# Performance work log

Measured on AMD Instinct MI355X. Metric: run time of the kernel, lower is better.

Reference implementation:

```python
import jax, jax.numpy as jnp
import numpy as np

B, N, E = 2, 4096, 256
H, TAU = 8, 32
HD = E // H
SCALING = HD ** -0.5


def setup_inputs() -> dict:
    key0 = jax.random.key(0)
    kq, kk, kv, kw = jax.random.split(key0, 4)
    return {
        "query": jax.random.normal(kq, (B, N, E), dtype=jnp.float32),
        "key": jax.random.normal(kk, (B, N, E), dtype=jnp.float32),
        "value": jax.random.normal(kv, (B, N, E), dtype=jnp.float32),
        "W": jax.random.normal(kw, (E, E), dtype=jnp.float32) * 0.02,
        "b": jnp.zeros((E,), dtype=jnp.float32),
    }


def reference(query, key, value, W, b):
    b_, n_, e_ = query.shape
    # Zero-pad the front so token i attends to keys/values at positions
    # [i - TAU + 1, ..., i] (sliding causal window of length TAU).
    pad = jnp.zeros((b_, TAU - 1, e_), dtype=query.dtype)
    kp = jnp.concatenate([pad, key], axis=1)   # [B, N+TAU-1, E]
    vp = jnp.concatenate([pad, value], axis=1)
    win_idx = jnp.arange(n_)[:, None] + jnp.arange(TAU)[None, :]  # [N, TAU]
    wk = kp[:, win_idx]  # [B, N, TAU, E] (materialized windows, as torch unfold does)
    wv = vp[:, win_idx]

    proj = lambda x: x @ W.T + b  # shared projection for q, k, v (single nn.Linear)
    q = proj(query).reshape(b_, n_, H, HD)            # [B, N, H, HD]
    k = proj(wk).reshape(b_, n_, TAU, H, HD)          # [B, N, TAU, H, HD]
    v = proj(wv).reshape(b_, n_, TAU, H, HD)

    scores = jnp.einsum("bnhd,bnthd->bhnt", q, k) * SCALING  # [B, H, N, TAU]
    attn = jax.nn.softmax(scores, axis=-1)
    out = jnp.einsum("bhnt,bnthd->bnhd", attn, v)             # [B, N, H, HD]
    return out.reshape(b_, n_, e_)
```

## Files before the change

kernel.cpp:

```cpp
#include <hip/hip_runtime.h>

#define SCALING 0.17677669529663687f

typedef __attribute__((ext_vector_type(8))) short bf8;
typedef __attribute__((ext_vector_type(4))) short bf4;
typedef __attribute__((ext_vector_type(4))) float floatx4;

__device__ __forceinline__ short f2bf(float f) {
    union { float f; unsigned u; } v; v.f = f;
    unsigned u = v.u;
    return (short)((u + 0x7FFFu + ((u >> 16) & 1u)) >> 16);
}
__device__ __forceinline__ float bf2f(short s) {
    union { unsigned u; float f; } v;
    v.u = ((unsigned)(unsigned short)s) << 16;
    return v.f;
}

#define PSTR 264
#define MSTR 36

__global__ __launch_bounds__(512, 2) void fused_kernel(
    const float* __restrict__ q, const float* __restrict__ k,
    const float* __restrict__ v, const float* __restrict__ W,
    const float* __restrict__ bias, float* __restrict__ out)
{
    __shared__ short Pl[160][PSTR];
    __shared__ short As[160][40];
    __shared__ short Bs[256][40];
    __shared__ float Mg[256][MSTR];

    const int tid = threadIdx.x;
    const int n0  = blockIdx.x * 32;
    const int b   = blockIdx.y;
    const int lane = tid & 63, wid = tid >> 6;
    const int wm = wid & 1, wn = wid >> 1;
    const int quad = lane >> 4, l16 = lane & 15;

    int a_row[3]; int a_c4[3]; const float* a_ptr[3];
    #pragma unroll
    for (int i = 0; i < 3; i++) {
        int idx = tid + i * 512;
        if (idx < 1280) {
            int r = idx >> 3;
            a_row[i] = r;
            a_c4[i]  = (idx & 7) * 4;
            const float* p;
            if (r < 32) {
                p = q + (size_t)(b * 4096 + n0 + r) * 256;
            } else if (r < 96) {
                int j = n0 + r - 64;
                p = (j >= 0) ? (k + (size_t)(b * 4096 + j) * 256) : nullptr;
            } else {
                int j = n0 + r - 128;
                p = (j >= 0) ? (v + (size_t)(b * 4096 + j) * 256) : nullptr;
            }
            a_ptr[i] = p;
        } else { a_row[i] = -1; a_c4[i] = 0; a_ptr[i] = nullptr; }
    }
    int w_row[4], w_c4[4];
    #pragma unroll
    for (int i = 0; i < 4; i++) {
        int idx = tid + i * 512;
        w_row[i] = idx >> 3;
        w_c4[i]  = (idx & 7) * 4;
    }

    floatx4 acc[5][4];
    #pragma unroll
    for (int mt = 0; mt < 5; mt++)
        #pragma unroll
        for (int nt = 0; nt < 4; nt++) acc[mt][nt] = (floatx4)0.0f;

    for (int k0 = 0; k0 < 256; k0 += 32) {
        bf4 ab[3];
        #pragma unroll
        for (int i = 0; i < 3; i++) {
            float4 xa = make_float4(0.f, 0.f, 0.f, 0.f);
            if (a_ptr[i]) xa = *(const float4*)(a_ptr[i] + k0 + a_c4[i]);
            ab[i][0] = f2bf(xa.x); ab[i][1] = f2bf(xa.y);
            ab[i][2] = f2bf(xa.z); ab[i][3] = f2bf(xa.w);
        }
        bf4 wb[4];
        #pragma unroll
        for (int i = 0; i < 4; i++) {
            float4 wv = *(const float4*)(W + (size_t)w_row[i] * 256 + k0 + w_c4[i]);
            wb[i][0] = f2bf(wv.x); wb[i][1] = f2bf(wv.y);
            wb[i][2] = f2bf(wv.z); wb[i][3] = f2bf(wv.w);
        }
        __syncthreads();
        #pragma unroll
        for (int i = 0; i < 3; i++)
            if (a_row[i] >= 0) *(bf4*)&As[a_row[i]][a_c4[i]] = ab[i];
        #pragma unroll
        for (int i = 0; i < 4; i++)
            *(bf4*)&Bs[w_row[i]][w_c4[i]] = wb[i];
        __syncthreads();

        bf8 af[5], bfr[4];
        #pragma unroll
        for (int mt = 0; mt < 5; mt++)
            af[mt] = *(const bf8*)&As[wm * 80 + mt * 16 + l16][quad * 8];
        #pragma unroll
        for (int nt = 0; nt < 4; nt++)
            bfr[nt] = *(const bf8*)&Bs[wn * 64 + nt * 16 + l16][quad * 8];
        #pragma unroll
        for (int mt = 0; mt < 5; mt++)
            #pragma unroll
            for (int nt = 0; nt < 4; nt++)
                acc[mt][nt] = __builtin_amdgcn_mfma_f32_16x16x32_bf16(
                    af[mt], bfr[nt], acc[mt][nt], 0, 0, 0);
    }

    #pragma unroll
    for (int nt = 0; nt < 4; nt++) {
        int col = wn * 64 + nt * 16 + l16;
        float bv = bias[col];
        #pragma unroll
        for (int mt = 0; mt < 5; mt++) {
            int rb = wm * 80 + mt * 16 + quad * 4;
            #pragma unroll
            for (int r = 0; r < 4; r++)
                Pl[rb + r][col] = f2bf(acc[mt][nt][r] + bv);
        }
    }
    __syncthreads();

    const int pid  = tid & 255;
    const int half = tid >> 8;
    const int nl   = pid & 31;
    const int h    = pid >> 5;
    const int cb   = h * 32;
    const int t0   = half * 16;

    float qv[32];
    #pragma unroll
    for (int c = 0; c < 4; c++) {
        bf8 t = *(const bf8*)&Pl[nl][cb + c * 8];
        #pragma unroll
        for (int e = 0; e < 8; e++) qv[c * 8 + e] = bf2f(t[e]);
    }

    float s[16], m = -3.0e38f;
    #pragma unroll
    for (int tt = 0; tt < 16; tt++) {
        int r = 33 + nl + t0 + tt;
        float a = 0.f;
        #pragma unroll
        for (int c = 0; c < 4; c++) {
            bf8 kk = *(const bf8*)&Pl[r][cb + c * 8];
            #pragma unroll
            for (int e = 0; e < 8; e++) a += qv[c * 8 + e] * bf2f(kk[e]);
        }
        s[tt] = a * SCALING;
        m = fmaxf(m, s[tt]);
    }
    float l = 0.f;
    #pragma unroll
    for (int tt = 0; tt < 16; tt++) { s[tt] = __expf(s[tt] - m); l += s[tt]; }

    float o[32];
    #pragma unroll
    for (int e = 0; e < 32; e++) o[e] = 0.f;
    #pragma unroll
    for (int tt = 0; tt < 16; tt++) {
        int r = 97 + nl + t0 + tt;
        float a = s[tt];
        #pragma unroll
        for (int c = 0; c < 4; c++) {
            bf8 vv = *(const bf8*)&Pl[r][cb + c * 8];
            #pragma unroll
            for (int e = 0; e < 8; e++) o[c * 8 + e] += a * bf2f(vv[e]);
        }
    }

    if (half == 1) {
        #pragma unroll
        for (int c = 0; c < 16; c++)
            *(float2*)&Mg[pid][c * 2] = make_float2(o[c * 2], o[c * 2 + 1]);
        Mg[pid][32] = m; Mg[pid][33] = l;
    }
    __syncthreads();
    if (half == 0) {
        float m1 = Mg[pid][32], l1 = Mg[pid][33];
        float mm = fmaxf(m, m1);
        float a0 = __expf(m - mm), a1 = __expf(m1 - mm);
        float inv = 1.0f / (a0 * l + a1 * l1);
        #pragma unroll
        for (int c = 0; c < 16; c++) {
            float2 o1 = *(const float2*)&Mg[pid][c * 2];
            float2 r2 = make_float2((a0 * o[c * 2]     + a1 * o1.x) * inv,
                                    (a0 * o[c * 2 + 1] + a1 * o1.y) * inv);
            *(float2*)&Mg[pid][c * 2] = r2;
        }
    }
    __syncthreads();

    const size_t obase = ((size_t)b * 4096 + n0) * 256;
    #pragma unroll
    for (int i = 0; i < 4; i++) {
        int t4   = tid + i * 512;
        int e    = t4 * 4;
        int n    = e >> 8;
        int rest = e & 255;
        int hh   = rest >> 5, cc = rest & 31;
        int pp   = hh * 32 + n;
        float4 val = *(const float4*)&Mg[pp][cc];
        *(float4*)(out + obase + (size_t)n * 256 + rest) = val;
    }
}

extern "C" void kernel_launch(void* const* d_in, const int* in_sizes, int n_in,
                              void* d_out, int out_size, void* d_ws, size_t ws_size,
                              hipStream_t stream) {
    (void)in_sizes; (void)n_in; (void)out_size; (void)d_ws; (void)ws_size;
    const float* q    = (const float*)d_in[0];
    const float* k    = (const float*)d_in[1];
    const float* v    = (const float*)d_in[2];
    const float* W    = (const float*)d_in[3];
    const float* bias = (const float*)d_in[4];
    float* outp = (float*)d_out;

    hipLaunchKernelGGL(fused_kernel, dim3(128, 2), dim3(512), 0, stream,
                       q, k, v, W, bias, outp);
}
```

Baseline: 97.14 us.

## Compute windowed attention scores and PV with MFMA instead of scalar loops

Replaces the per-thread scalar QK dot products and PV accumulation with MFMA tiles per head (one wave per head). Scores are computed as banded 32x64 block products with masking, softmax is reduced via lane shuffles, probabilities are staged in fp16 shared memory, and V is stored transposed in fp16 for an fp16 MFMA. Scaling is folded into Q at projection time and the merge buffer and its syncs are removed. This trades redundant masked MFMA work and an fp16 precision change for far fewer scalar FMAs and LDS reads.

```diff
diff --git a/kernel.cpp b/kernel.cpp
--- a/kernel.cpp
+++ b/kernel.cpp
@@ -4,6 +4,8 @@
 
 typedef __attribute__((ext_vector_type(8))) short bf8;
 typedef __attribute__((ext_vector_type(4))) short bf4;
+typedef _Float16 half8 __attribute__((ext_vector_type(8)));
+typedef _Float16 half4 __attribute__((ext_vector_type(4)));
 typedef __attribute__((ext_vector_type(4))) float floatx4;
 
 __device__ __forceinline__ short f2bf(float f) {
@@ -11,24 +13,20 @@
     unsigned u = v.u;
     return (short)((u + 0x7FFFu + ((u >> 16) & 1u)) >> 16);
 }
-__device__ __forceinline__ float bf2f(short s) {
-    union { unsigned u; float f; } v;
-    v.u = ((unsigned)(unsigned short)s) << 16;
-    return v.f;
-}
 
 #define PSTR 264
-#define MSTR 36
+#define VSTR 72
 
 __global__ __launch_bounds__(512, 2) void fused_kernel(
     const float* __restrict__ q, const float* __restrict__ k,
     const float* __restrict__ v, const float* __restrict__ W,
     const float* __restrict__ bias, float* __restrict__ out)
 {
-    __shared__ short Pl[160][PSTR];
-    __shared__ short As[160][40];
-    __shared__ short Bs[256][40];
-    __shared__ float Mg[256][MSTR];
+    __shared__ short    Pl[96][PSTR];
+    __shared__ _Float16 Vt[256][VSTR];
+    __shared__ _Float16 Ps[8][32][VSTR];
+    __shared__ short    As[160][40];
+    __shared__ short    Bs[256][40];
 
     const int tid = threadIdx.x;
     const int n0  = blockIdx.x * 32;
@@ -119,95 +117,122 @@
         #pragma unroll
         for (int mt = 0; mt < 5; mt++) {
             int rb = wm * 80 + mt * 16 + quad * 4;
-            #pragma unroll
-            for (int r = 0; r < 4; r++)
-                Pl[rb + r][col] = f2bf(acc[mt][nt][r] + bv);
+            if (rb < 96) {
+                const bool isQ = (rb < 32);
+                #pragma unroll
+                for (int r = 0; r < 4; r++) {
+                    float val = acc[mt][nt][r] + bv;
+                    Pl[rb + r][col] = f2bf(isQ ? val * SCALING : val);
+                }
+            } else {
+                half4 hv;
+                #pragma unroll
+                for (int r = 0; r < 4; r++) hv[r] = (_Float16)(acc[mt][nt][r] + bv);
+                *(half4*)&Vt[col][rb - 96] = hv;
+            }
         }
     }
     __syncthreads();
 
-    const int pid  = tid & 255;
-    const int half = tid >> 8;
-    const int nl   = pid & 31;
-    const int h    = pid >> 5;
-    const int cb   = h * 32;
-    const int t0   = half * 16;
-
-    float qv[32];
-    #pragma unroll
-    for (int c = 0; c < 4; c++) {
-        bf8 t = *(const bf8*)&Pl[nl][cb + c * 8];
-        #pragma unroll
-        for (int e = 0; e < 8; e++) qv[c * 8 + e] = bf2f(t[e]);
-    }
-
-    float s[16], m = -3.0e38f;
-    #pragma unroll
-    for (int tt = 0; tt < 16; tt++) {
-        int r = 33 + nl + t0 + tt;
-        float a = 0.f;
-        #pragma unroll
-        for (int c = 0; c < 4; c++) {
-            bf8 kk = *(const bf8*)&Pl[r][cb + c * 8];
-            #pragma unroll
-            for (int e = 0; e < 8; e++) a += qv[c * 8 + e] * bf2f(kk[e]);
-        }
-        s[tt] = a * SCALING;
-        m = fmaxf(m, s[tt]);
-    }
-    float l = 0.f;
-    #pragma unroll
-    for (int tt = 0; tt < 16; tt++) { s[tt] = __expf(s[tt] - m); l += s[tt]; }
-
-    float o[32];
-    #pragma unroll
-    for (int e = 0; e < 32; e++) o[e] = 0.f;
-    #pragma unroll
-    for (int tt = 0; tt < 16; tt++) {
-        int r = 97 + nl + t0 + tt;
-        float a = s[tt];
-        #pragma unroll
-        for (int c = 0; c < 4; c++) {
-            bf8 vv = *(const bf8*)&Pl[r][cb + c * 8];
-            #pragma unroll
-            for (int e = 0; e < 8; e++) o[c * 8 + e] += a * bf2f(vv[e]);
-        }
-    }
-
-    if (half == 1) {
-        #pragma unroll
-        for (int c = 0; c < 16; c++)
-            *(float2*)&Mg[pid][c * 2] = make_float2(o[c * 2], o[c * 2 + 1]);
-        Mg[pid][32] = m; Mg[pid][33] = l;
-    }
-    __syncthreads();
-    if (half == 0) {
-        float m1 = Mg[pid][32], l1 = Mg[pid][33];
-        float mm = fmaxf(m, m1);
-        float a0 = __expf(m - mm), a1 = __expf(m1 - mm);
-        float inv = 1.0f / (a0 * l + a1 * l1);
-        #pragma unroll
-        for (int c = 0; c < 16; c++) {
-            float2 o1 = *(const float2*)&Mg[pid][c * 2];
-            float2 r2 = make_float2((a0 * o[c * 2]     + a1 * o1.x) * inv,
-                                    (a0 * o[c * 2 + 1] + a1 * o1.y) * inv);
-            *(float2*)&Mg[pid][c * 2] = r2;
-        }
-    }
-    __syncthreads();
+    const int h  = wid;
+    const int cb = h * 32;
+
+    bf8 qf[2], kf[4];
+    #pragma unroll
+    for (int mt = 0; mt < 2; mt++)
+        qf[mt] = *(const bf8*)&Pl[mt * 16 + l16][cb + quad * 8];
+    #pragma unroll
+    for (int jt = 0; jt < 4; jt++)
+        kf[jt] = *(const bf8*)&Pl[32 + jt * 16 + l16][cb + quad * 8];
+
+    floatx4 S[2][4];
+    S[0][0] = __builtin_amdgcn_mfma_f32_16x16x32_bf16(qf[0], kf[0], (floatx4)0.f, 0, 0, 0);
+    S[0][1] = __builtin_amdgcn_mfma_f32_16x16x32_bf16(qf[0], kf[1], (floatx4)0.f, 0, 0, 0);
+    S[0][2] = __builtin_amdgcn_mfma_f32_16x16x32_bf16(qf[0], kf[2], (floatx4)0.f, 0, 0, 0);
+    S[1][1] = __builtin_amdgcn_mfma_f32_16x16x32_bf16(qf[1], kf[1], (floatx4)0.f, 0, 0, 0);
+    S[1][2] = __builtin_amdgcn_mfma_f32_16x16x32_bf16(qf[1], kf[2], (floatx4)0.f, 0, 0, 0);
+    S[1][3] = __builtin_amdgcn_mfma_f32_16x16x32_bf16(qf[1], kf[3], (floatx4)0.f, 0, 0, 0);
+
+    float p[2][3][4], inv[2][4];
+    #pragma unroll
+    for (int mt = 0; mt < 2; mt++) {
+        #pragma unroll
+        for (int r = 0; r < 4; r++) {
+            int n = mt * 16 + quad * 4 + r;
+            float sv[3], mx = -3.0e38f;
+            #pragma unroll
+            for (int u = 0; u < 3; u++) {
+                int i = (u + mt) * 16 + l16;
+                bool valid = (i > n) && (i <= n + 32);
+                sv[u] = valid ? S[mt][u + mt][r] : -3.0e38f;
+                mx = fmaxf(mx, sv[u]);
+            }
+            #pragma unroll
+            for (int off = 1; off < 16; off <<= 1)
+                mx = fmaxf(mx, __shfl_xor(mx, off, 64));
+            float lsum = 0.f;
+            #pragma unroll
+            for (int u = 0; u < 3; u++) {
+                float pv = (sv[u] > -1.0e38f) ? __expf(sv[u] - mx) : 0.f;
+                p[mt][u][r] = pv;
+                lsum += pv;
+            }
+            #pragma unroll
+            for (int off = 1; off < 16; off <<= 1)
+                lsum += __shfl_xor(lsum, off, 64);
+            inv[mt][r] = 1.0f / lsum;
+        }
+    }
+
+    _Float16 (*myPs)[VSTR] = Ps[h];
+    #pragma unroll
+    for (int mt = 0; mt < 2; mt++) {
+        int zjt = (mt == 0) ? 3 : 0;
+        #pragma unroll
+        for (int r = 0; r < 4; r++) {
+            int row = mt * 16 + quad * 4 + r;
+            #pragma unroll
+            for (int u = 0; u < 3; u++)
+                myPs[row][(u + mt) * 16 + l16] = (_Float16)p[mt][u][r];
+            myPs[row][zjt * 16 + l16] = (_Float16)0.f;
+        }
+    }
+
+    half8 pf[2][2], vf[2][2];
+    #pragma unroll
+    for (int mt = 0; mt < 2; mt++)
+        #pragma unroll
+        for (int ks = 0; ks < 2; ks++)
+            pf[mt][ks] = *(const half8*)&myPs[mt * 16 + l16][ks * 32 + quad * 8];
+    #pragma unroll
+    for (int dt = 0; dt < 2; dt++)
+        #pragma unroll
+        for (int ks = 0; ks < 2; ks++)
+            vf[dt][ks] = *(const half8*)&Vt[cb + dt * 16 + l16][ks * 32 + quad * 8];
+
+    floatx4 O[2][2];
+    #pragma unroll
+    for (int mt = 0; mt < 2; mt++)
+        #pragma unroll
+        for (int dt = 0; dt < 2; dt++) {
+            O[mt][dt] = (floatx4)0.f;
+            #pragma unroll
+            for (int ks = 0; ks < 2; ks++)
+                O[mt][dt] = __builtin_amdgcn_mfma_f32_16x16x32_f16(
+                    pf[mt][ks], vf[dt][ks], O[mt][dt], 0, 0, 0);
+        }
 
     const size_t obase = ((size_t)b * 4096 + n0) * 256;
     #pragma unroll
-    for (int i = 0; i < 4; i++) {
-        int t4   = tid + i * 512;
-        int e    = t4 * 4;
-        int n    = e >> 8;
-        int rest = e & 255;
-        int hh   = rest >> 5, cc = rest & 31;
-        int pp   = hh * 32 + n;
-        float4 val = *(const float4*)&Mg[pp][cc];
-        *(float4*)(out + obase + (size_t)n * 256 + rest) = val;
-    }
+    for (int mt = 0; mt < 2; mt++)
+        #pragma unroll
+        for (int dt = 0; dt < 2; dt++)
+            #pragma unroll
+            for (int r = 0; r < 4; r++) {
+                int n = mt * 16 + quad * 4 + r;
+                out[obase + (size_t)n * 256 + cb + dt * 16 + l16] =
+                    O[mt][dt][r] * inv[mt][r];
+            }
 }
 
 extern "C" void kernel_launch(void* const* d_in, const int* in_sizes, int n_in,
```

Result: faster. 91.97 us (median of 2 runs) (-5.3%).
